# Kernel optimization log

Measured on AMD Instinct MI355X. Metric: run time of the kernel, lower is better.

Reference implementation:

```python
import jax, jax.numpy as jnp
import numpy as np

B, N, DIM, H = 2, 2048, 1024, 16
HD = DIM // H
SCALE = HD ** -0.5


def setup_inputs() -> dict:
    key = jax.random.key(0)
    ks = jax.random.split(key, 11)
    std = DIM ** -0.5
    inp = {
        'q': jax.random.normal(ks[0], (B, N, DIM), jnp.float32),
        'k': jax.random.normal(ks[1], (B, N, DIM), jnp.float32),
        'v': jax.random.normal(ks[2], (B, N, DIM), jnp.float32),
        # causal mask, broadcast over batch and heads; mask==0 -> masked out
        'mask': jnp.tril(jnp.ones((N, N), jnp.int32))[None, None],
        'Wq': jax.random.normal(ks[3], (DIM, DIM), jnp.float32) * std,
        'bq': jnp.zeros((DIM,), jnp.float32),
        'Wk': jax.random.normal(ks[4], (DIM, DIM), jnp.float32) * std,
        'bk': jnp.zeros((DIM,), jnp.float32),
        'Wv': jax.random.normal(ks[5], (DIM, DIM), jnp.float32) * std,
        'bv': jnp.zeros((DIM,), jnp.float32),
        'Wo': jax.random.normal(ks[6], (DIM, DIM), jnp.float32) * std,
        'bo': jnp.zeros((DIM,), jnp.float32),
    }
    return inp


def _split_heads(x):  # [b, n, dim] -> [b, h, n, c]
    b, n, _ = x.shape
    return x.reshape(b, n, H, HD).transpose(0, 2, 1, 3)


def reference(q, k, v, mask, Wq, bq, Wk, bk, Wv, bv, Wo, bo):
    qh = _split_heads(q @ Wq.T + bq)                      # [b,h,nq,c]
    kh = _split_heads(k @ Wk.T + bk)                      # [b,h,nk,c]
    vh = _split_heads(v @ Wv.T + bv)                      # [b,h,nk,c]
    attn = jnp.einsum('bhqc,bhkc->bhqk', qh, kh) * SCALE  # [b,h,nq,nk]
    attn = jnp.where(mask == 0, -jnp.inf, attn)
    attn = jax.nn.softmax(attn, axis=-1)
    out = jnp.einsum('bhqk,bhkc->bhqc', attn, vh)          # [b,h,nq,c]
    b, h, n, c = out.shape
    out = out.transpose(0, 2, 1, 3).reshape(b, n, h * c)   # [b,nq,dim]
    return out @ Wo.T + bo
```

## Files before the change

### kernel.cpp

```cpp
#include <hip/hip_runtime.h>

#define NN 2048
#define DIMD 1024
#define HH 16
#define HDD 64
#define SC2 0.1803368801111244f

typedef __attribute__((ext_vector_type(8))) short bf16x8;
typedef __attribute__((ext_vector_type(4))) float f32x4;
typedef unsigned short ushort_t;
typedef unsigned int uint_t;

__device__ __forceinline__ ushort_t f2bf(float f) {
    union { float f; uint_t u; } v; v.f = f;
    uint_t u = v.u;
    return (ushort_t)((u + 0x7FFFu + ((u >> 16) & 1u)) >> 16);
}
__device__ __forceinline__ ushort_t f2bf_trunc(float f) {
    union { float f; uint_t u; } v; v.f = f;
    return (ushort_t)(v.u >> 16);
}
__device__ __forceinline__ void gl_lds16(const ushort_t* g, ushort_t* l) {
    __builtin_amdgcn_global_load_lds(
        (const __attribute__((address_space(1))) void*)g,
        (__attribute__((address_space(3))) void*)l, 16, 0, 0);
}

__global__ __launch_bounds__(256) void convert_k(
    const float* __restrict__ q, const float* __restrict__ k, const float* __restrict__ v,
    const float* __restrict__ wq, const float* __restrict__ wk,
    const float* __restrict__ wv, const float* __restrict__ wo,
    ushort_t* __restrict__ Abf, ushort_t* __restrict__ Wbf) {
    size_t gid = (size_t)blockIdx.x * 256 + threadIdx.x;
    size_t e = gid * 8;
    const float* src; ushort_t* dst;
    float sc = 1.f;
    if (e < 12582912) {
        int i = (int)(e >> 22);
        src = (i == 0 ? q : (i == 1 ? k : v)) + (e & 4194303);
        dst = Abf + e;
    } else {
        size_t e2 = e - 12582912;
        int i = (int)(e2 >> 20);
        src = (i == 0 ? wq : (i == 1 ? wk : (i == 2 ? wv : wo))) + (e2 & 1048575);
        dst = Wbf + e2;
        if (i == 0) sc = SC2;
    }
    float4 x = ((const float4*)src)[0], y = ((const float4*)src)[1];
    union { uint4 u; ushort_t s[8]; } pk;
    pk.s[0] = f2bf(x.x * sc); pk.s[1] = f2bf(x.y * sc); pk.s[2] = f2bf(x.z * sc); pk.s[3] = f2bf(x.w * sc);
    pk.s[4] = f2bf(y.x * sc); pk.s[5] = f2bf(y.y * sc); pk.s[6] = f2bf(y.z * sc); pk.s[7] = f2bf(y.w * sc);
    *(uint4*)dst = pk.u;
}

template<int MODE>
__global__ __launch_bounds__(256) void gemm_k(
    const ushort_t* __restrict__ Abase, const ushort_t* __restrict__ Wbase,
    const float* __restrict__ b0p, const float* __restrict__ b1p, const float* __restrict__ b2p,
    ushort_t* __restrict__ d0, ushort_t* __restrict__ d1, ushort_t* __restrict__ d2,
    float* __restrict__ fout) {
    const int K = 1024;
    __shared__ ushort_t As[2][128 * 32];
    __shared__ ushort_t Bs[2][128 * 32];
    int z = (MODE == 0) ? blockIdx.z : 0;
    const ushort_t* A = Abase + (size_t)z * 4096 * 1024;
    const ushort_t* W = Wbase + (size_t)z * 1024 * 1024;
    const float* bias = (MODE == 0) ? (z == 0 ? b0p : (z == 1 ? b1p : b2p)) : b0p;
    int tid = threadIdx.x;
    int m0 = blockIdx.x * 128, n0 = blockIdx.y * 128;
    int lane = tid & 63, wave = tid >> 6;
    int quad = lane >> 4, l15 = lane & 15;
    int wm = (wave >> 1) * 64, wn = (wave & 1) * 64;

    f32x4 acc[4][4];
    for (int i = 0; i < 4; i++)
        for (int j = 0; j < 4; j++)
            acc[i][j] = (f32x4){0.f, 0.f, 0.f, 0.f};

    int r0 = tid >> 2, cg0 = tid & 3;
    int r1 = (tid + 256) >> 2, cg1 = tid & 3;

    gl_lds16(A + (size_t)(m0 + r0) * K + cg0 * 8, &As[0][(0 * 256 + wave * 64) * 8]);
    gl_lds16(W + (size_t)(n0 + r0) * K + cg0 * 8, &Bs[0][(0 * 256 + wave * 64) * 8]);
    gl_lds16(A + (size_t)(m0 + r1) * K + cg1 * 8, &As[0][(1 * 256 + wave * 64) * 8]);
    gl_lds16(W + (size_t)(n0 + r1) * K + cg1 * 8, &Bs[0][(1 * 256 + wave * 64) * 8]);

    for (int it = 0; it < 32; it++) {
        int cur = it & 1;
        __syncthreads();
        if (it < 31) {
            int k0 = (it + 1) * 32, nb = 1 - cur;
            gl_lds16(A + (size_t)(m0 + r0) * K + k0 + cg0 * 8, &As[nb][(0 * 256 + wave * 64) * 8]);
            gl_lds16(W + (size_t)(n0 + r0) * K + k0 + cg0 * 8, &Bs[nb][(0 * 256 + wave * 64) * 8]);
            gl_lds16(A + (size_t)(m0 + r1) * K + k0 + cg1 * 8, &As[nb][(1 * 256 + wave * 64) * 8]);
            gl_lds16(W + (size_t)(n0 + r1) * K + k0 + cg1 * 8, &Bs[nb][(1 * 256 + wave * 64) * 8]);
        }
        bf16x8 a[4], b[4];
        for (int mt = 0; mt < 4; mt++)
            a[mt] = *(const bf16x8*)&As[cur][(wm + mt * 16 + l15) * 32 + quad * 8];
        for (int nt = 0; nt < 4; nt++)
            b[nt] = *(const bf16x8*)&Bs[cur][(wn + nt * 16 + l15) * 32 + quad * 8];
        for (int mt = 0; mt < 4; mt++)
            for (int nt = 0; nt < 4; nt++)
                acc[mt][nt] = __builtin_amdgcn_mfma_f32_16x16x32_bf16(a[mt], b[nt], acc[mt][nt], 0, 0, 0);
    }
    for (int nt = 0; nt < 4; nt++) {
        int n = n0 + wn + nt * 16 + l15;
        float bv = bias[n];
        if (MODE == 0 && z == 0) bv *= SC2;
        for (int mt = 0; mt < 4; mt++)
            for (int r = 0; r < 4; r++) {
                int m = m0 + wm + mt * 16 + quad * 4 + r;
                float val = acc[mt][nt][r] + bv;
                if (MODE == 0) {
                    int b = m >> 11, ns = m & 2047;
                    int h = n >> 6, c = n & 63;
                    if (z == 2)
                        d2[(((size_t)(b * HH + h)) * HDD + c) * NN + ns] = f2bf(val);
                    else {
                        ushort_t* dst = (z == 0) ? d0 : d1;
                        dst[(((size_t)(b * HH + h)) * NN + ns) * HDD + c] = f2bf(val);
                    }
                } else {
                    fout[(size_t)m * DIMD + n] = val;
                }
            }
    }
}

__global__ __launch_bounds__(256, 4) void attn4(const ushort_t* __restrict__ Qh,
                                                const ushort_t* __restrict__ Kh,
                                                const ushort_t* __restrict__ VtG,
                                                ushort_t* __restrict__ aout) {
    __shared__ ushort_t Kb[2][64 * 64];
    __shared__ ushort_t Vb[2][64 * 64];
    __shared__ ushort_t Ps[4][16 * 64];
    int tid = threadIdx.x, lane = tid & 63, w = tid >> 6;
    int quad = lane >> 4, l15 = lane & 15;
    int bh = blockIdx.y;
    int x = blockIdx.x;
    int qb = (x & 1) ? (31 - (x >> 1)) : (x >> 1);
    const ushort_t* Qp = Qh + (size_t)bh * NN * HDD;
    const ushort_t* Kp = Kh + (size_t)bh * NN * HDD;
    const ushort_t* Vp = VtG + (size_t)bh * HDD * NN;
    int row_lo = qb * 64 + w * 16;

    bf16x8 aq[2];
    for (int kc = 0; kc < 2; kc++)
        aq[kc] = *(const bf16x8*)&Qp[(size_t)(row_lo + l15) * HDD + kc * 32 + quad * 8];

    f32x4 o[4];
    float l_acc[4];
    for (int ct = 0; ct < 4; ct++) o[ct] = (f32x4){0.f, 0.f, 0.f, 0.f};
    for (int r = 0; r < 4; r++) l_acc[r] = 0.f;

    int sr0 = tid >> 3, scg0 = tid & 7;
    int sr1 = (tid + 256) >> 3, scg1 = tid & 7;
    int ssc0 = scg0 ^ (sr0 & 7);
    int ssc1 = scg1 ^ (sr1 & 7);

    int key = l15 & 7;
    int c0 = (quad ^ key) * 8;
    int c1 = ((4 + quad) ^ key) * 8;

    {
        gl_lds16(Kp + sr0 * 64 + ssc0 * 8, &Kb[0][(0 * 256 + w * 64) * 8]);
        gl_lds16(Kp + sr1 * 64 + ssc1 * 8, &Kb[0][(1 * 256 + w * 64) * 8]);
        gl_lds16(Vp + (size_t)sr0 * NN + ssc0 * 8, &Vb[0][(0 * 256 + w * 64) * 8]);
        gl_lds16(Vp + (size_t)sr1 * NN + ssc1 * 8, &Vb[0][(1 * 256 + w * 64) * 8]);
    }

    for (int kb = 0; kb <= qb; kb++) {
        int cur = kb & 1;
        __syncthreads();
        if (kb < qb) {
            int nb = 1 - cur, kn = kb + 1;
            gl_lds16(Kp + (size_t)(kn * 64 + sr0) * 64 + ssc0 * 8, &Kb[nb][(0 * 256 + w * 64) * 8]);
            gl_lds16(Kp + (size_t)(kn * 64 + sr1) * 64 + ssc1 * 8, &Kb[nb][(1 * 256 + w * 64) * 8]);
            gl_lds16(Vp + (size_t)sr0 * NN + kn * 64 + ssc0 * 8, &Vb[nb][(0 * 256 + w * 64) * 8]);
            gl_lds16(Vp + (size_t)sr1 * NN + kn * 64 + ssc1 * 8, &Vb[nb][(1 * 256 + w * 64) * 8]);
        }

        f32x4 s[4];
        for (int nt = 0; nt < 4; nt++) {
            bf16x8 b0 = *(const bf16x8*)&Kb[cur][(nt * 16 + l15) * 64 + c0];
            bf16x8 b1 = *(const bf16x8*)&Kb[cur][(nt * 16 + l15) * 64 + c1];
            f32x4 zz = (f32x4){0.f, 0.f, 0.f, 0.f};
            zz = __builtin_amdgcn_mfma_f32_16x16x32_bf16(aq[0], b0, zz, 0, 0, 0);
            s[nt] = __builtin_amdgcn_mfma_f32_16x16x32_bf16(aq[1], b1, zz, 0, 0, 0);
        }
        if (kb == qb) {
            for (int nt = 0; nt < 4; nt++)
                for (int r = 0; r < 4; r++) {
                    int kv = kb * 64 + nt * 16 + l15;
                    int qq = row_lo + quad * 4 + r;
                    float p = (kv <= qq) ? exp2f(s[nt][r]) : 0.f;
                    s[nt][r] = p;
                    l_acc[r] += p;
                }
        } else {
            for (int nt = 0; nt < 4; nt++)
                for (int r = 0; r < 4; r++) {
                    float p = exp2f(s[nt][r]);
                    s[nt][r] = p;
                    l_acc[r] += p;
                }
        }
        for (int nt = 0; nt < 4; nt++)
            for (int r = 0; r < 4; r++) {
                int qr = quad * 4 + r;
                int cc = (nt * 2 + (l15 >> 3)) ^ (qr & 7);
                Ps[w][qr * 64 + cc * 8 + (l15 & 7)] = f2bf_trunc(s[nt][r]);
            }
        bf16x8 ap0 = *(const bf16x8*)&Ps[w][l15 * 64 + c0];
        bf16x8 ap1 = *(const bf16x8*)&Ps[w][l15 * 64 + c1];
        for (int ct = 0; ct < 4; ct++) {
            bf16x8 bv0 = *(const bf16x8*)&Vb[cur][(ct * 16 + l15) * 64 + c0];
            bf16x8 bv1 = *(const bf16x8*)&Vb[cur][(ct * 16 + l15) * 64 + c1];
            o[ct] = __builtin_amdgcn_mfma_f32_16x16x32_bf16(ap0, bv0, o[ct], 0, 0, 0);
            o[ct] = __builtin_amdgcn_mfma_f32_16x16x32_bf16(ap1, bv1, o[ct], 0, 0, 0);
        }
    }
    float rl[4];
    for (int r = 0; r < 4; r++) {
        float t = l_acc[r];
        for (int d = 1; d < 16; d <<= 1) t += __shfl_xor(t, d);
        rl[r] = 1.f / t;
    }
    int b = bh >> 4, h = bh & 15;
    for (int ct = 0; ct < 4; ct++)
        for (int r = 0; r < 4; r++) {
            int qq = row_lo + quad * 4 + r;
            int c = ct * 16 + l15;
            aout[((size_t)(b * NN + qq)) * DIMD + h * HDD + c] = f2bf(o[ct][r] * rl[r]);
        }
}

extern "C" void kernel_launch(void* const* d_in, const int* in_sizes, int n_in,
                              void* d_out, int out_size, void* d_ws, size_t ws_size,
                              hipStream_t stream) {
    const float* q  = (const float*)d_in[0];
    const float* k  = (const float*)d_in[1];
    const float* v  = (const float*)d_in[2];
    const float* Wq = (const float*)d_in[4];
    const float* bq = (const float*)d_in[5];
    const float* Wk = (const float*)d_in[6];
    const float* bk = (const float*)d_in[7];
    const float* Wv = (const float*)d_in[8];
    const float* bv = (const float*)d_in[9];
    const float* Wo = (const float*)d_in[10];
    const float* bo = (const float*)d_in[11];
    float* out = (float*)d_out;

    char* ws = (char*)d_ws;
    ushort_t* Abf  = (ushort_t*)(ws);
    ushort_t* Wbf  = (ushort_t*)(ws + (24ull << 20));
    ushort_t* Qh   = (ushort_t*)(ws + (32ull << 20));
    ushort_t* Kh   = (ushort_t*)(ws + (40ull << 20));
    ushort_t* VtG  = (ushort_t*)(ws + (48ull << 20));
    ushort_t* AObf = (ushort_t*)(ws + (56ull << 20));

    hipLaunchKernelGGL(convert_k, dim3(8192), dim3(256), 0, stream,
                       q, k, v, Wq, Wk, Wv, Wo, Abf, Wbf);
    hipLaunchKernelGGL((gemm_k<0>), dim3(32, 8, 3), dim3(256), 0, stream,
                       Abf, Wbf, bq, bk, bv, Qh, Kh, VtG, (float*)nullptr);
    hipLaunchKernelGGL(attn4, dim3(32, 32), dim3(256), 0, stream, Qh, Kh, VtG, AObf);
    hipLaunchKernelGGL((gemm_k<1>), dim3(32, 8, 1), dim3(256), 0, stream,
                       AObf, Wbf + 3ull * 1024 * 1024, bo, nullptr, nullptr,
                       nullptr, nullptr, nullptr, out);
}
```

Before: 258.6 us.

## Pair causal query blocks per workgroup and keep P in registers via transposed S

Each attention workgroup now handles two query blocks (qa and 31-qa) that share the same K/V tiles loaded to LDS, which balances causal work per block and halves K/V traffic. S is computed transposed (K as A operand) so the probabilities land in the register layout needed for an fp16 16x16x16 MFMA with V. This removes the LDS round trip through the P buffer. V is now written in fp16 by the projection GEMM with packed 8-byte stores. The cost is fp16 precision for V and P, more registers (launch bounds lowered to 2), and half as many blocks in the grid.

New measurement: 250.4 us. 3.2% less time.

```diff
diff --git a/kernel.cpp b/kernel.cpp
--- a/kernel.cpp
+++ b/kernel.cpp
@@ -8,17 +8,17 @@
 
 typedef __attribute__((ext_vector_type(8))) short bf16x8;
 typedef __attribute__((ext_vector_type(4))) float f32x4;
+typedef __attribute__((ext_vector_type(4))) _Float16 f16x4;
 typedef unsigned short ushort_t;
 typedef unsigned int uint_t;
+
+#define MFMA32(a, b, c) __builtin_amdgcn_mfma_f32_16x16x32_bf16((a), (b), (c), 0, 0, 0)
+#define MFMA16H(a, b, c) __builtin_amdgcn_mfma_f32_16x16x16f16((a), (b), (c), 0, 0, 0)
 
 __device__ __forceinline__ ushort_t f2bf(float f) {
     union { float f; uint_t u; } v; v.f = f;
     uint_t u = v.u;
     return (ushort_t)((u + 0x7FFFu + ((u >> 16) & 1u)) >> 16);
-}
-__device__ __forceinline__ ushort_t f2bf_trunc(float f) {
-    union { float f; uint_t u; } v; v.f = f;
-    return (ushort_t)(v.u >> 16);
 }
 __device__ __forceinline__ void gl_lds16(const ushort_t* g, ushort_t* l) {
     __builtin_amdgcn_global_load_lds(
@@ -102,138 +102,180 @@
             b[nt] = *(const bf16x8*)&Bs[cur][(wn + nt * 16 + l15) * 32 + quad * 8];
         for (int mt = 0; mt < 4; mt++)
             for (int nt = 0; nt < 4; nt++)
-                acc[mt][nt] = __builtin_amdgcn_mfma_f32_16x16x32_bf16(a[mt], b[nt], acc[mt][nt], 0, 0, 0);
-    }
-    for (int nt = 0; nt < 4; nt++) {
-        int n = n0 + wn + nt * 16 + l15;
-        float bv = bias[n];
-        if (MODE == 0 && z == 0) bv *= SC2;
-        for (int mt = 0; mt < 4; mt++)
-            for (int r = 0; r < 4; r++) {
-                int m = m0 + wm + mt * 16 + quad * 4 + r;
-                float val = acc[mt][nt][r] + bv;
-                if (MODE == 0) {
-                    int b = m >> 11, ns = m & 2047;
-                    int h = n >> 6, c = n & 63;
-                    if (z == 2)
-                        d2[(((size_t)(b * HH + h)) * HDD + c) * NN + ns] = f2bf(val);
-                    else {
+                acc[mt][nt] = MFMA32(a[mt], b[nt], acc[mt][nt]);
+    }
+    if (MODE == 0 && z == 2) {
+        for (int nt = 0; nt < 4; nt++) {
+            int n = n0 + wn + nt * 16 + l15;
+            float bv = bias[n];
+            int h = n >> 6, c = n & 63;
+            for (int mt = 0; mt < 4; mt++) {
+                int mb = m0 + wm + mt * 16 + quad * 4;
+                int b = mb >> 11, ns = mb & 2047;
+                union { uint2 u2; _Float16 hh[4]; } pkv;
+                pkv.hh[0] = (_Float16)(acc[mt][nt][0] + bv);
+                pkv.hh[1] = (_Float16)(acc[mt][nt][1] + bv);
+                pkv.hh[2] = (_Float16)(acc[mt][nt][2] + bv);
+                pkv.hh[3] = (_Float16)(acc[mt][nt][3] + bv);
+                *(uint2*)&d2[(((size_t)(b * HH + h)) * HDD + c) * NN + ns] = pkv.u2;
+            }
+        }
+    } else {
+        for (int nt = 0; nt < 4; nt++) {
+            int n = n0 + wn + nt * 16 + l15;
+            float bv = bias[n];
+            if (MODE == 0 && z == 0) bv *= SC2;
+            for (int mt = 0; mt < 4; mt++)
+                for (int r = 0; r < 4; r++) {
+                    int m = m0 + wm + mt * 16 + quad * 4 + r;
+                    float val = acc[mt][nt][r] + bv;
+                    if (MODE == 0) {
+                        int b = m >> 11, ns = m & 2047;
+                        int h = n >> 6, c = n & 63;
                         ushort_t* dst = (z == 0) ? d0 : d1;
                         dst[(((size_t)(b * HH + h)) * NN + ns) * HDD + c] = f2bf(val);
-                    }
-                } else {
-                    fout[(size_t)m * DIMD + n] = val;
+                    } else {
+                        fout[(size_t)m * DIMD + n] = val;
+                    }
                 }
-            }
-    }
-}
-
-__global__ __launch_bounds__(256, 4) void attn4(const ushort_t* __restrict__ Qh,
+        }
+    }
+}
+
+__global__ __launch_bounds__(256, 2) void attn5(const ushort_t* __restrict__ Qh,
                                                 const ushort_t* __restrict__ Kh,
                                                 const ushort_t* __restrict__ VtG,
                                                 ushort_t* __restrict__ aout) {
     __shared__ ushort_t Kb[2][64 * 64];
     __shared__ ushort_t Vb[2][64 * 64];
-    __shared__ ushort_t Ps[4][16 * 64];
     int tid = threadIdx.x, lane = tid & 63, w = tid >> 6;
     int quad = lane >> 4, l15 = lane & 15;
     int bh = blockIdx.y;
-    int x = blockIdx.x;
-    int qb = (x & 1) ? (31 - (x >> 1)) : (x >> 1);
+    int qa = blockIdx.x;
+    int qc = 31 - qa;
     const ushort_t* Qp = Qh + (size_t)bh * NN * HDD;
     const ushort_t* Kp = Kh + (size_t)bh * NN * HDD;
     const ushort_t* Vp = VtG + (size_t)bh * HDD * NN;
-    int row_lo = qb * 64 + w * 16;
-
-    bf16x8 aq[2];
-    for (int kc = 0; kc < 2; kc++)
-        aq[kc] = *(const bf16x8*)&Qp[(size_t)(row_lo + l15) * HDD + kc * 32 + quad * 8];
-
-    f32x4 o[4];
-    float l_acc[4];
-    for (int ct = 0; ct < 4; ct++) o[ct] = (f32x4){0.f, 0.f, 0.f, 0.f};
-    for (int r = 0; r < 4; r++) l_acc[r] = 0.f;
-
-    int sr0 = tid >> 3, scg0 = tid & 7;
-    int sr1 = (tid + 256) >> 3, scg1 = tid & 7;
-    int ssc0 = scg0 ^ (sr0 & 7);
-    int ssc1 = scg1 ^ (sr1 & 7);
-
+    int ra = qa * 64 + w * 16;
+    int rc = qc * 64 + w * 16;
+
+    bf16x8 aqa[2], aqc[2];
+    for (int kc = 0; kc < 2; kc++) {
+        aqa[kc] = *(const bf16x8*)&Qp[(size_t)(ra + l15) * HDD + kc * 32 + quad * 8];
+        aqc[kc] = *(const bf16x8*)&Qp[(size_t)(rc + l15) * HDD + kc * 32 + quad * 8];
+    }
+
+    f32x4 oa[4], oc[4];
+    for (int ct = 0; ct < 4; ct++) {
+        oa[ct] = (f32x4){0.f, 0.f, 0.f, 0.f};
+        oc[ct] = (f32x4){0.f, 0.f, 0.f, 0.f};
+    }
+    float la = 0.f, lc = 0.f;
+
+    int sr0 = tid >> 3, scg = tid & 7;
+    int sr1 = sr0 + 32;
+    int ssc = scg ^ (sr0 & 7);
     int key = l15 & 7;
     int c0 = (quad ^ key) * 8;
     int c1 = ((4 + quad) ^ key) * 8;
 
-    {
-        gl_lds16(Kp + sr0 * 64 + ssc0 * 8, &Kb[0][(0 * 256 + w * 64) * 8]);
-        gl_lds16(Kp + sr1 * 64 + ssc1 * 8, &Kb[0][(1 * 256 + w * 64) * 8]);
-        gl_lds16(Vp + (size_t)sr0 * NN + ssc0 * 8, &Vb[0][(0 * 256 + w * 64) * 8]);
-        gl_lds16(Vp + (size_t)sr1 * NN + ssc1 * 8, &Vb[0][(1 * 256 + w * 64) * 8]);
-    }
-
-    for (int kb = 0; kb <= qb; kb++) {
+    gl_lds16(Kp + (size_t)sr0 * 64 + ssc * 8, &Kb[0][(0 * 256 + w * 64) * 8]);
+    gl_lds16(Kp + (size_t)sr1 * 64 + ssc * 8, &Kb[0][(1 * 256 + w * 64) * 8]);
+    gl_lds16(Vp + (size_t)sr0 * NN + ssc * 8, &Vb[0][(0 * 256 + w * 64) * 8]);
+    gl_lds16(Vp + (size_t)sr1 * NN + ssc * 8, &Vb[0][(1 * 256 + w * 64) * 8]);
+
+    for (int kb = 0; kb <= qc; kb++) {
         int cur = kb & 1;
         __syncthreads();
-        if (kb < qb) {
+        if (kb < qc) {
             int nb = 1 - cur, kn = kb + 1;
-            gl_lds16(Kp + (size_t)(kn * 64 + sr0) * 64 + ssc0 * 8, &Kb[nb][(0 * 256 + w * 64) * 8]);
-            gl_lds16(Kp + (size_t)(kn * 64 + sr1) * 64 + ssc1 * 8, &Kb[nb][(1 * 256 + w * 64) * 8]);
-            gl_lds16(Vp + (size_t)sr0 * NN + kn * 64 + ssc0 * 8, &Vb[nb][(0 * 256 + w * 64) * 8]);
-            gl_lds16(Vp + (size_t)sr1 * NN + kn * 64 + ssc1 * 8, &Vb[nb][(1 * 256 + w * 64) * 8]);
-        }
-
-        f32x4 s[4];
+            gl_lds16(Kp + (size_t)(kn * 64 + sr0) * 64 + ssc * 8, &Kb[nb][(0 * 256 + w * 64) * 8]);
+            gl_lds16(Kp + (size_t)(kn * 64 + sr1) * 64 + ssc * 8, &Kb[nb][(1 * 256 + w * 64) * 8]);
+            gl_lds16(Vp + (size_t)sr0 * NN + kn * 64 + ssc * 8, &Vb[nb][(0 * 256 + w * 64) * 8]);
+            gl_lds16(Vp + (size_t)sr1 * NN + kn * 64 + ssc * 8, &Vb[nb][(1 * 256 + w * 64) * 8]);
+        }
+        bool da = (kb <= qa);
+
+        bf16x8 kf0[4], kf1[4];
         for (int nt = 0; nt < 4; nt++) {
-            bf16x8 b0 = *(const bf16x8*)&Kb[cur][(nt * 16 + l15) * 64 + c0];
-            bf16x8 b1 = *(const bf16x8*)&Kb[cur][(nt * 16 + l15) * 64 + c1];
-            f32x4 zz = (f32x4){0.f, 0.f, 0.f, 0.f};
-            zz = __builtin_amdgcn_mfma_f32_16x16x32_bf16(aq[0], b0, zz, 0, 0, 0);
-            s[nt] = __builtin_amdgcn_mfma_f32_16x16x32_bf16(aq[1], b1, zz, 0, 0, 0);
-        }
-        if (kb == qb) {
+            kf0[nt] = *(const bf16x8*)&Kb[cur][(nt * 16 + l15) * 64 + c0];
+            kf1[nt] = *(const bf16x8*)&Kb[cur][(nt * 16 + l15) * 64 + c1];
+        }
+        f16x4 vf[4][4];
+        for (int ct = 0; ct < 4; ct++)
             for (int nt = 0; nt < 4; nt++)
-                for (int r = 0; r < 4; r++) {
-                    int kv = kb * 64 + nt * 16 + l15;
-                    int qq = row_lo + quad * 4 + r;
-                    float p = (kv <= qq) ? exp2f(s[nt][r]) : 0.f;
-                    s[nt][r] = p;
-                    l_acc[r] += p;
-                }
-        } else {
-            for (int nt = 0; nt < 4; nt++)
-                for (int r = 0; r < 4; r++) {
-                    float p = exp2f(s[nt][r]);
-                    s[nt][r] = p;
-                    l_acc[r] += p;
-                }
-        }
-        for (int nt = 0; nt < 4; nt++)
-            for (int r = 0; r < 4; r++) {
-                int qr = quad * 4 + r;
-                int cc = (nt * 2 + (l15 >> 3)) ^ (qr & 7);
-                Ps[w][qr * 64 + cc * 8 + (l15 & 7)] = f2bf_trunc(s[nt][r]);
-            }
-        bf16x8 ap0 = *(const bf16x8*)&Ps[w][l15 * 64 + c0];
-        bf16x8 ap1 = *(const bf16x8*)&Ps[w][l15 * 64 + c1];
+                vf[ct][nt] = *(const f16x4*)&Vb[cur][(ct * 16 + l15) * 64 +
+                                ((2 * nt + (quad >> 1)) ^ key) * 8 + (quad & 1) * 4];
+
+        {
+            f32x4 s[4];
+            for (int nt = 0; nt < 4; nt++) {
+                f32x4 z = (f32x4){0.f, 0.f, 0.f, 0.f};
+                z = MFMA32(kf0[nt], aqc[0], z);
+                s[nt] = MFMA32(kf1[nt], aqc[1], z);
+            }
+            f16x4 ap[4];
+            if (kb == qc) {
+                for (int nt = 0; nt < 4; nt++)
+                    for (int r = 0; r < 4; r++) {
+                        int kv = kb * 64 + nt * 16 + quad * 4 + r;
+                        float p = (kv <= rc + l15) ? exp2f(s[nt][r]) : 0.f;
+                        ap[nt][r] = (_Float16)p; lc += p;
+                    }
+            } else {
+                for (int nt = 0; nt < 4; nt++)
+                    for (int r = 0; r < 4; r++) {
+                        float p = exp2f(s[nt][r]);
+                        ap[nt][r] = (_Float16)p; lc += p;
+                    }
+            }
+            for (int ct = 0; ct < 4; ct++)
+                for (int nt = 0; nt < 4; nt++)
+                    oc[ct] = MFMA16H(ap[nt], vf[ct][nt], oc[ct]);
+        }
+        if (da) {
+            f32x4 s[4];
+            for (int nt = 0; nt < 4; nt++) {
+                f32x4 z = (f32x4){0.f, 0.f, 0.f, 0.f};
+                z = MFMA32(kf0[nt], aqa[0], z);
+                s[nt] = MFMA32(kf1[nt], aqa[1], z);
+            }
+            f16x4 ap[4];
+            if (kb == qa) {
+                for (int nt = 0; nt < 4; nt++)
+                    for (int r = 0; r < 4; r++) {
+                        int kv = kb * 64 + nt * 16 + quad * 4 + r;
+                        float p = (kv <= ra + l15) ? exp2f(s[nt][r]) : 0.f;
+                        ap[nt][r] = (_Float16)p; la += p;
+                    }
+            } else {
+                for (int nt = 0; nt < 4; nt++)
+                    for (int r = 0; r < 4; r++) {
+                        float p = exp2f(s[nt][r]);
+                        ap[nt][r] = (_Float16)p; la += p;
+                    }
+            }
+            for (int ct = 0; ct < 4; ct++)
+                for (int nt = 0; nt < 4; nt++)
+                    oa[ct] = MFMA16H(ap[nt], vf[ct][nt], oa[ct]);
+        }
+    }
+
+    la += __shfl_xor(la, 16); la += __shfl_xor(la, 32);
+    lc += __shfl_xor(lc, 16); lc += __shfl_xor(lc, 32);
+
+    int b = bh >> 4, h = bh & 15;
+    for (int r = 0; r < 4; r++) {
+        float ila = 1.f / __shfl(la, quad * 4 + r);
+        float ilc = 1.f / __shfl(lc, quad * 4 + r);
         for (int ct = 0; ct < 4; ct++) {
-            bf16x8 bv0 = *(const bf16x8*)&Vb[cur][(ct * 16 + l15) * 64 + c0];
-            bf16x8 bv1 = *(const bf16x8*)&Vb[cur][(ct * 16 + l15) * 64 + c1];
-            o[ct] = __builtin_amdgcn_mfma_f32_16x16x32_bf16(ap0, bv0, o[ct], 0, 0, 0);
-            o[ct] = __builtin_amdgcn_mfma_f32_16x16x32_bf16(ap1, bv1, o[ct], 0, 0, 0);
-        }
-    }
-    float rl[4];
-    for (int r = 0; r < 4; r++) {
-        float t = l_acc[r];
-        for (int d = 1; d < 16; d <<= 1) t += __shfl_xor(t, d);
-        rl[r] = 1.f / t;
-    }
-    int b = bh >> 4, h = bh & 15;
-    for (int ct = 0; ct < 4; ct++)
-        for (int r = 0; r < 4; r++) {
-            int qq = row_lo + quad * 4 + r;
             int c = ct * 16 + l15;
-            aout[((size_t)(b * NN + qq)) * DIMD + h * HDD + c] = f2bf(o[ct][r] * rl[r]);
-        }
+            int qqa = ra + quad * 4 + r;
+            int qqc = rc + quad * 4 + r;
+            aout[((size_t)(b * NN + qqa)) * DIMD + h * HDD + c] = f2bf(oa[ct][r] * ila);
+            aout[((size_t)(b * NN + qqc)) * DIMD + h * HDD + c] = f2bf(oc[ct][r] * ilc);
+        }
+    }
 }
 
 extern "C" void kernel_launch(void* const* d_in, const int* in_sizes, int n_in,
@@ -264,7 +306,7 @@
                        q, k, v, Wq, Wk, Wv, Wo, Abf, Wbf);
     hipLaunchKernelGGL((gemm_k<0>), dim3(32, 8, 3), dim3(256), 0, stream,
                        Abf, Wbf, bq, bk, bv, Qh, Kh, VtG, (float*)nullptr);
-    hipLaunchKernelGGL(attn4, dim3(32, 32), dim3(256), 0, stream, Qh, Kh, VtG, AObf);
+    hipLaunchKernelGGL(attn5, dim3(16, 32), dim3(256), 0, stream, Qh, Kh, VtG, AObf);
     hipLaunchKernelGGL((gemm_k<1>), dim3(32, 8, 1), dim3(256), 0, stream,
                        AObf, Wbf + 3ull * 1024 * 1024, bo, nullptr, nullptr,
                        nullptr, nullptr, nullptr, out);
```
